# Optimization experiments

Measured on AMD Instinct MI355X. Metric: run time of the kernel, lower is better.

The kernel has to match this reference:

```python
import jax, jax.numpy as jnp
import numpy as np

B, D, M = 32, 640, 1024
EPS = 1e-05


def setup_inputs() -> dict:
    key = jax.random.key(0)
    x = jax.random.normal(key, (B, D, M), dtype=jnp.float32)
    return {"x": x}


def _triu_flat_indices(d):
    iu, ju = np.triu_indices(d)
    return jnp.asarray(iu * d + ju, dtype=jnp.int32)


def reference(x):
    b, d, m = x.shape
    # Gram matrix: x @ x^T  -> [b, d, d]
    x_pow2 = jnp.einsum('bim,bjm->bij', x, x)
    # I_M @ (x_pow2 * I) + (x_pow2 * I) @ I_M - 2*x_pow2
    # (x_pow2 * I) is diagonal, so ones-matrix bmm = broadcast of the diagonal.
    diag = jnp.diagonal(x_pow2, axis1=1, axis2=2)  # [b, d]
    dcov = diag[:, None, :] + diag[:, :, None] - 2.0 * x_pow2
    dcov = jnp.maximum(dcov, 0.0)
    # temperature param is built in-forward: exp(log(1/(2*d*m))) = 1/(2*d*m)
    temperature = 1.0 / (2.0 * d * m)
    dcov = jnp.sqrt(temperature * dcov + EPS)
    # Double centering: dcov @ I_M = row sums broadcast; I_M @ dcov = col sums.
    row_mean = dcov.sum(axis=2, keepdims=True) / d          # [b, d, 1]
    col_mean = dcov.sum(axis=1, keepdims=True) / d          # [b, 1, d]
    tot_mean = dcov.sum(axis=(1, 2), keepdims=True) / (d * d)
    t = dcov - row_mean - col_mean + tot_mean               # [b, d, d]
    # Triuvec: gather upper-triangular entries (incl. diagonal)
    flat_idx = _triu_flat_indices(d)                         # [d*(d+1)//2]
    y = t.reshape(b, d * d)[:, flat_idx]
    return y
```

## Files before the change

kernel.cpp:

```cpp
#include <hip/hip_runtime.h>

#define D_DIM 640
#define M_DIM 1024
#define B_DIM 32
#define BK 32
#define OUT_ROW 205120

typedef __bf16 bf16x8 __attribute__((ext_vector_type(8)));
typedef float f32x4 __attribute__((ext_vector_type(4)));

__device__ __forceinline__ unsigned short f2bf(float f) {
    union { float f; unsigned int u; } c; c.f = f;
    unsigned int u = c.u;
    unsigned int r = (u + 0x7fffu + ((u >> 16) & 1u)) >> 16;
    return (unsigned short)r;
}

__device__ __forceinline__ float bf2f(unsigned short h) {
    union { unsigned int u; float f; } c; c.u = ((unsigned int)h) << 16;
    return c.f;
}

__device__ __forceinline__ void gload_lds16(const unsigned short* g, unsigned short* l) {
    __builtin_amdgcn_global_load_lds(
        (const __attribute__((address_space(1))) unsigned int*)g,
        (__attribute__((address_space(3))) unsigned int*)l,
        16, 0, 0);
}

__device__ __forceinline__ float block_reduce_256(float s) {
    #pragma unroll
    for (int off = 32; off > 0; off >>= 1) s += __shfl_down(s, off, 64);
    __shared__ float red[4];
    if ((threadIdx.x & 63) == 0) red[threadIdx.x >> 6] = s;
    __syncthreads();
    return red[0] + red[1] + red[2] + red[3];
}

__global__ void cast_diag_kernel(const float* __restrict__ x,
                                 unsigned short* __restrict__ xb,
                                 float* __restrict__ diag,
                                 float* __restrict__ rowsum,
                                 float* __restrict__ tot) {
    const size_t row = blockIdx.x;
    const int t = threadIdx.x;
    const float4 v = ((const float4*)(x + row * M_DIM))[t];
    float s = v.x * v.x + v.y * v.y + v.z * v.z + v.w * v.w;
    ushort4 o;
    o.x = f2bf(v.x); o.y = f2bf(v.y); o.z = f2bf(v.z); o.w = f2bf(v.w);
    ((ushort4*)(xb + row * M_DIM))[t] = o;
    float ssum = block_reduce_256(s);
    if (t == 0) { diag[row] = ssum; rowsum[row] = 0.f; }
    if (t == 1 && row < B_DIM) tot[row] = 0.f;
}

__global__ __launch_bounds__(256, 2)
void gemm_dcov_kernel(const unsigned short* __restrict__ xb,
                      const float* __restrict__ diag,
                      unsigned short* __restrict__ dcov,
                      float* __restrict__ rowsum,
                      float* __restrict__ tot) {
    __shared__ __align__(16) unsigned short smem[32768];

    const int id = blockIdx.x;
    const int bt = (id & 7) * 4 + ((id >> 3) & 3);
    int p = id >> 5;
    int it = 0, off = p;
    while (off >= 5 - it) { off -= 5 - it; ++it; }
    const int jt = it + off;
    const bool diagTile = (it == jt);

    const int tid = threadIdx.x;
    const int w = tid >> 6, l = tid & 63;
    const int wy = w >> 1, wx = w & 1;
    const int lm = l & 15, quad = l >> 4;

    const unsigned short* gA = xb + ((size_t)bt * D_DIM + it * 128) * M_DIM;
    const unsigned short* gB = xb + ((size_t)bt * D_DIM + jt * 128) * M_DIM;

    const int r0 = tid >> 2;
    const int cl = (((tid & 3) ^ ((tid >> 3) & 3)) << 3);
    const size_t aoff1 = (size_t)r0 * M_DIM + cl;
    const size_t aoff2 = aoff1 + (size_t)64 * M_DIM;
    const int ldst = tid * 8;

    auto issue = [&](int k, int ph) {
        unsigned short* sA = smem + ph * 8192;
        unsigned short* sB = sA + 4096;
        const int koff = k * BK;
        gload_lds16(gA + aoff1 + koff, sA + ldst);
        gload_lds16(gA + aoff2 + koff, sA + ldst + 2048);
        gload_lds16(gB + aoff1 + koff, sB + ldst);
        gload_lds16(gB + aoff2 + koff, sB + ldst + 2048);
    };

    f32x4 acc[4][4];
    const f32x4 zero = {0.f, 0.f, 0.f, 0.f};
    #pragma unroll
    for (int i = 0; i < 4; i++)
        #pragma unroll
        for (int j = 0; j < 4; j++) acc[i][j] = zero;

    const int sw = ((quad ^ ((lm >> 1) & 3)) << 3);

    issue(0, 0); issue(1, 1); issue(2, 2);

    int ph = 0;
    for (int k = 0; k < 32; ++k) {
        if (k < 30)       asm volatile("s_waitcnt vmcnt(8)" ::: "memory");
        else if (k == 30) asm volatile("s_waitcnt vmcnt(4)" ::: "memory");
        else              asm volatile("s_waitcnt vmcnt(0)" ::: "memory");
        asm volatile("s_barrier" ::: "memory");
        if (k + 3 < 32) issue(k + 3, (ph + 3) & 3);

        const unsigned short* sA = smem + ph * 8192;
        const unsigned short* sB = sA + 4096;
        bf16x8 af[4], bfr[4];
        #pragma unroll
        for (int mi = 0; mi < 4; mi++)
            af[mi] = *(const bf16x8*)&sA[(wy * 64 + mi * 16 + lm) * BK + sw];
        #pragma unroll
        for (int ni = 0; ni < 4; ni++)
            bfr[ni] = *(const bf16x8*)&sB[(wx * 64 + ni * 16 + lm) * BK + sw];

        #pragma unroll
        for (int mi = 0; mi < 4; mi++)
            #pragma unroll
            for (int ni = 0; ni < 4; ni++)
                acc[mi][ni] = __builtin_amdgcn_mfma_f32_16x16x32_bf16(
                    af[mi], bfr[ni], acc[mi][ni], 0, 0, 0);

        ph = (ph + 1) & 3;
    }

    float* sd = (float*)smem;
    if (tid < 128) sd[tid] = diag[(size_t)bt * D_DIM + it * 128 + tid];
    else           sd[tid] = diag[(size_t)bt * D_DIM + jt * 128 + (tid - 128)];
    __syncthreads();

    const float temp = 7.62939453125e-07f;
    unsigned short* dbase = dcov + (size_t)bt * D_DIM * D_DIM;
    float* rs = rowsum + (size_t)bt * D_DIM;
    float ts = 0.f;
    float cp[4] = {0.f, 0.f, 0.f, 0.f};

    #pragma unroll
    for (int mi = 0; mi < 4; mi++) {
        #pragma unroll
        for (int r = 0; r < 4; r++) {
            const int lrow = wy * 64 + mi * 16 + quad * 4 + r;
            const int grow = it * 128 + lrow;
            const float di = sd[lrow];
            float rp = 0.f;
            #pragma unroll
            for (int ni = 0; ni < 4; ni++) {
                const int lcol = wx * 64 + ni * 16 + lm;
                const int gcol = jt * 128 + lcol;
                const float dj = sd[128 + lcol];
                const float g = acc[mi][ni][r];
                const float v = sqrtf(fmaf(temp, fmaxf(di + dj - 2.f * g, 0.f), 1e-5f));
                dbase[(size_t)grow * D_DIM + gcol] = f2bf(v);
                rp += v;
                cp[ni] += v;
            }
            ts += rp;
            rp += __shfl_down(rp, 8, 16);
            rp += __shfl_down(rp, 4, 16);
            rp += __shfl_down(rp, 2, 16);
            rp += __shfl_down(rp, 1, 16);
            if (lm == 0) atomicAdd(&rs[grow], rp);
        }
    }
    if (!diagTile) {
        #pragma unroll
        for (int ni = 0; ni < 4; ni++) {
            float c = cp[ni];
            c += __shfl_down(c, 32);
            c += __shfl_down(c, 16);
            if (l < 16) atomicAdd(&rs[jt * 128 + wx * 64 + ni * 16 + lm], c);
        }
    }
    float bs = block_reduce_256(ts);
    if (tid == 0) atomicAdd(&tot[bt], diagTile ? bs : 2.f * bs);
}

__global__ void output_kernel(const unsigned short* __restrict__ dcov,
                              const float* __restrict__ rowsum,
                              const float* __restrict__ tot,
                              float* __restrict__ out) {
    const int b = blockIdx.x / D_DIM;
    const int i = blockIdx.x - b * D_DIM;
    const float inv_d = 1.f / (float)D_DIM;
    const float rmi = rowsum[(size_t)b * D_DIM + i] * inv_d;
    const float tm = tot[b] * (inv_d * inv_d);
    const unsigned short* drow = dcov + ((size_t)b * D_DIM + i) * D_DIM;
    const float* rs = rowsum + (size_t)b * D_DIM;
    float* orow = out + (size_t)b * OUT_ROW + (size_t)i * D_DIM - (size_t)i * (i - 1) / 2;
    for (int j = i + threadIdx.x; j < D_DIM; j += 256)
        orow[j - i] = bf2f(drow[j]) - rmi - rs[j] * inv_d + tm;
}

extern "C" void kernel_launch(void* const* d_in, const int* in_sizes, int n_in,
                              void* d_out, int out_size, void* d_ws, size_t ws_size,
                              hipStream_t stream) {
    const float* x = (const float*)d_in[0];
    float* out = (float*)d_out;

    char* ws = (char*)d_ws;
    unsigned short* xb = (unsigned short*)ws;
    size_t off = 41943040;
    float* diag = (float*)(ws + off);           off += 81920;
    unsigned short* dcov = (unsigned short*)(ws + off); off += 26214400;
    float* rowsum = (float*)(ws + off);         off += 81920;
    float* tot = (float*)(ws + off);            off += 256;

    cast_diag_kernel<<<dim3(B_DIM * D_DIM), 256, 0, stream>>>(x, xb, diag, rowsum, tot);
    gemm_dcov_kernel<<<dim3(480), 256, 0, stream>>>(xb, diag, dcov, rowsum, tot);
    output_kernel<<<dim3(B_DIM * D_DIM), 256, 0, stream>>>(dcov, rowsum, tot, out);
}
```

Measured before the change: 171.5 us.

## Shrink GEMM tiles to 64x64 with 32x32x16 MFMA for more blocks

Cuts the Gram tile from 128x128 to 64x64, so each batch has 55 upper-triangular tile pairs instead of 15, and switches each wave to a single 32x32x16 bf16 MFMA accumulator. The grid grows from 480 to 1760 blocks, LDS per block is halved, and launch bounds now allow 4 blocks per CU, all aimed at better occupancy and CU utilization. The epilogue's row and column reductions are rewritten for the new accumulator layout. In exchange, each tile has lower arithmetic intensity, each block redundantly loads more operand data, and there are more atomics on the row sums.

After: 191.1 us. 11.4% more time.

```diff
diff --git a/kernel.cpp b/kernel.cpp
--- a/kernel.cpp
+++ b/kernel.cpp
@@ -4,10 +4,13 @@
 #define M_DIM 1024
 #define B_DIM 32
 #define BK 32
+#define TILE 64
+#define NT 10
+#define NPAIR 55
 #define OUT_ROW 205120
 
 typedef __bf16 bf16x8 __attribute__((ext_vector_type(8)));
-typedef float f32x4 __attribute__((ext_vector_type(4)));
+typedef float f32x16 __attribute__((ext_vector_type(16)));
 
 __device__ __forceinline__ unsigned short f2bf(float f) {
     union { float f; unsigned int u; } c; c.f = f;
@@ -54,131 +57,107 @@
     if (t == 1 && row < B_DIM) tot[row] = 0.f;
 }
 
-__global__ __launch_bounds__(256, 2)
+__global__ __launch_bounds__(256, 4)
 void gemm_dcov_kernel(const unsigned short* __restrict__ xb,
                       const float* __restrict__ diag,
                       unsigned short* __restrict__ dcov,
                       float* __restrict__ rowsum,
                       float* __restrict__ tot) {
-    __shared__ __align__(16) unsigned short smem[32768];
+    __shared__ __align__(16) unsigned short smem[16384];
 
     const int id = blockIdx.x;
-    const int bt = (id & 7) * 4 + ((id >> 3) & 3);
+    const int sub = id & 31;
+    const int bt = (sub & 7) * 4 + (sub >> 3);
     int p = id >> 5;
     int it = 0, off = p;
-    while (off >= 5 - it) { off -= 5 - it; ++it; }
+    while (off >= NT - it) { off -= NT - it; ++it; }
     const int jt = it + off;
     const bool diagTile = (it == jt);
 
     const int tid = threadIdx.x;
     const int w = tid >> 6, l = tid & 63;
     const int wy = w >> 1, wx = w & 1;
-    const int lm = l & 15, quad = l >> 4;
+    const int lr = l & 31;
+    const int lk = l >> 5;
 
-    const unsigned short* gA = xb + ((size_t)bt * D_DIM + it * 128) * M_DIM;
-    const unsigned short* gB = xb + ((size_t)bt * D_DIM + jt * 128) * M_DIM;
+    const unsigned short* gA = xb + ((size_t)bt * D_DIM + it * TILE) * M_DIM;
+    const unsigned short* gB = xb + ((size_t)bt * D_DIM + jt * TILE) * M_DIM;
 
-    const int r0 = tid >> 2;
     const int cl = (((tid & 3) ^ ((tid >> 3) & 3)) << 3);
-    const size_t aoff1 = (size_t)r0 * M_DIM + cl;
-    const size_t aoff2 = aoff1 + (size_t)64 * M_DIM;
+    const size_t aoff = (size_t)(tid >> 2) * M_DIM + cl;
     const int ldst = tid * 8;
 
     auto issue = [&](int k, int ph) {
-        unsigned short* sA = smem + ph * 8192;
-        unsigned short* sB = sA + 4096;
+        unsigned short* s = smem + ph * 4096;
         const int koff = k * BK;
-        gload_lds16(gA + aoff1 + koff, sA + ldst);
-        gload_lds16(gA + aoff2 + koff, sA + ldst + 2048);
-        gload_lds16(gB + aoff1 + koff, sB + ldst);
-        gload_lds16(gB + aoff2 + koff, sB + ldst + 2048);
+        gload_lds16(gA + aoff + koff, s + ldst);
+        gload_lds16(gB + aoff + koff, s + 2048 + ldst);
     };
 
-    f32x4 acc[4][4];
-    const f32x4 zero = {0.f, 0.f, 0.f, 0.f};
+    f32x16 acc;
     #pragma unroll
-    for (int i = 0; i < 4; i++)
-        #pragma unroll
-        for (int j = 0; j < 4; j++) acc[i][j] = zero;
+    for (int i = 0; i < 16; i++) acc[i] = 0.f;
 
-    const int sw = ((quad ^ ((lm >> 1) & 3)) << 3);
+    const int swz = (lr >> 1) & 3;
+    const int a0 = (wy * 32 + lr) * BK + (((lk) ^ swz) << 3);
+    const int a1 = (wy * 32 + lr) * BK + (((2 + lk) ^ swz) << 3);
+    const int b0 = 2048 + (wx * 32 + lr) * BK + (((lk) ^ swz) << 3);
+    const int b1 = 2048 + (wx * 32 + lr) * BK + (((2 + lk) ^ swz) << 3);
 
     issue(0, 0); issue(1, 1); issue(2, 2);
 
     int ph = 0;
     for (int k = 0; k < 32; ++k) {
-        if (k < 30)       asm volatile("s_waitcnt vmcnt(8)" ::: "memory");
-        else if (k == 30) asm volatile("s_waitcnt vmcnt(4)" ::: "memory");
+        if (k < 30)       asm volatile("s_waitcnt vmcnt(4)" ::: "memory");
+        else if (k == 30) asm volatile("s_waitcnt vmcnt(2)" ::: "memory");
         else              asm volatile("s_waitcnt vmcnt(0)" ::: "memory");
         asm volatile("s_barrier" ::: "memory");
-        if (k + 3 < 32) issue(k + 3, (ph + 3) & 3);
+        if (k < 29) issue(k + 3, (ph + 3) & 3);
 
-        const unsigned short* sA = smem + ph * 8192;
-        const unsigned short* sB = sA + 4096;
-        bf16x8 af[4], bfr[4];
-        #pragma unroll
-        for (int mi = 0; mi < 4; mi++)
-            af[mi] = *(const bf16x8*)&sA[(wy * 64 + mi * 16 + lm) * BK + sw];
-        #pragma unroll
-        for (int ni = 0; ni < 4; ni++)
-            bfr[ni] = *(const bf16x8*)&sB[(wx * 64 + ni * 16 + lm) * BK + sw];
-
-        #pragma unroll
-        for (int mi = 0; mi < 4; mi++)
-            #pragma unroll
-            for (int ni = 0; ni < 4; ni++)
-                acc[mi][ni] = __builtin_amdgcn_mfma_f32_16x16x32_bf16(
-                    af[mi], bfr[ni], acc[mi][ni], 0, 0, 0);
+        const unsigned short* s = smem + ph * 4096;
+        bf16x8 fa0 = *(const bf16x8*)&s[a0];
+        bf16x8 fb0 = *(const bf16x8*)&s[b0];
+        bf16x8 fa1 = *(const bf16x8*)&s[a1];
+        bf16x8 fb1 = *(const bf16x8*)&s[b1];
+        acc = __builtin_amdgcn_mfma_f32_32x32x16_bf16(fa0, fb0, acc, 0, 0, 0);
+        acc = __builtin_amdgcn_mfma_f32_32x32x16_bf16(fa1, fb1, acc, 0, 0, 0);
 
         ph = (ph + 1) & 3;
     }
 
     float* sd = (float*)smem;
-    if (tid < 128) sd[tid] = diag[(size_t)bt * D_DIM + it * 128 + tid];
-    else           sd[tid] = diag[(size_t)bt * D_DIM + jt * 128 + (tid - 128)];
+    if (tid < TILE)           sd[tid] = diag[(size_t)bt * D_DIM + it * TILE + tid];
+    else if (tid < 2 * TILE)  sd[tid] = diag[(size_t)bt * D_DIM + jt * TILE + (tid - TILE)];
     __syncthreads();
 
     const float temp = 7.62939453125e-07f;
     unsigned short* dbase = dcov + (size_t)bt * D_DIM * D_DIM;
     float* rs = rowsum + (size_t)bt * D_DIM;
-    float ts = 0.f;
-    float cp[4] = {0.f, 0.f, 0.f, 0.f};
+    const int gcol = jt * TILE + wx * 32 + lr;
+    const float dj = sd[TILE + wx * 32 + lr];
+    float cp = 0.f;
 
     #pragma unroll
-    for (int mi = 0; mi < 4; mi++) {
-        #pragma unroll
-        for (int r = 0; r < 4; r++) {
-            const int lrow = wy * 64 + mi * 16 + quad * 4 + r;
-            const int grow = it * 128 + lrow;
-            const float di = sd[lrow];
-            float rp = 0.f;
-            #pragma unroll
-            for (int ni = 0; ni < 4; ni++) {
-                const int lcol = wx * 64 + ni * 16 + lm;
-                const int gcol = jt * 128 + lcol;
-                const float dj = sd[128 + lcol];
-                const float g = acc[mi][ni][r];
-                const float v = sqrtf(fmaf(temp, fmaxf(di + dj - 2.f * g, 0.f), 1e-5f));
-                dbase[(size_t)grow * D_DIM + gcol] = f2bf(v);
-                rp += v;
-                cp[ni] += v;
-            }
-            ts += rp;
-            rp += __shfl_down(rp, 8, 16);
-            rp += __shfl_down(rp, 4, 16);
-            rp += __shfl_down(rp, 2, 16);
-            rp += __shfl_down(rp, 1, 16);
-            if (lm == 0) atomicAdd(&rs[grow], rp);
-        }
+    for (int r = 0; r < 16; r++) {
+        const int row_local = (r & 3) + 8 * (r >> 2) + 4 * lk;
+        const int grow = it * TILE + wy * 32 + row_local;
+        const float di = sd[wy * 32 + row_local];
+        const float g = acc[r];
+        const float v = sqrtf(fmaf(temp, fmaxf(di + dj - 2.f * g, 0.f), 1e-5f));
+        dbase[(size_t)grow * D_DIM + gcol] = f2bf(v);
+        cp += v;
+        float rp = v;
+        rp += __shfl_down(rp, 16, 32);
+        rp += __shfl_down(rp, 8, 32);
+        rp += __shfl_down(rp, 4, 32);
+        rp += __shfl_down(rp, 2, 32);
+        rp += __shfl_down(rp, 1, 32);
+        if (lr == 0) atomicAdd(&rs[grow], rp);
     }
+    float ts = cp;
     if (!diagTile) {
-        #pragma unroll
-        for (int ni = 0; ni < 4; ni++) {
-            float c = cp[ni];
-            c += __shfl_down(c, 32);
-            c += __shfl_down(c, 16);
-            if (l < 16) atomicAdd(&rs[jt * 128 + wx * 64 + ni * 16 + lm], c);
-        }
+        float c = cp + __shfl_down(cp, 32);
+        if (l < 32) atomicAdd(&rs[gcol], c);
     }
     float bs = block_reduce_256(ts);
     if (tid == 0) atomicAdd(&tot[bt], diagTile ? bs : 2.f * bs);
@@ -215,6 +194,6 @@
     float* tot = (float*)(ws + off);            off += 256;
 
     cast_diag_kernel<<<dim3(B_DIM * D_DIM), 256, 0, stream>>>(x, xb, diag, rowsum, tot);
-    gemm_dcov_kernel<<<dim3(480), 256, 0, stream>>>(xb, diag, dcov, rowsum, tot);
+    gemm_dcov_kernel<<<dim3(NPAIR * B_DIM), 256, 0, stream>>>(xb, diag, dcov, rowsum, tot);
     output_kernel<<<dim3(B_DIM * D_DIM), 256, 0, stream>>>(dcov, rowsum, tot, out);
 }
```
